# Kernel tuning notes

Hardware: AMD Instinct MI355X
Metric: run time of the kernel (lower is better)

## Reference

```python
import jax, jax.numpy as jnp
import numpy as np

BETA = 0.25
NUM_BOOKS = 8
CODEBOOK_SIZE = 1024
CODEBOOK_DIM = 128
INPUT_DIM = 512


def setup_inputs() -> dict:
    key = jax.random.key(0)
    ks = jax.random.split(key, 6)
    B, T = 16, 4096
    z = jax.random.normal(ks[0], (B, INPUT_DIM, T), dtype=jnp.float32)
    W_in = jax.random.normal(ks[1], (CODEBOOK_DIM, INPUT_DIM), dtype=jnp.float32) * (1.0 / np.sqrt(INPUT_DIM))
    b_in = jax.random.normal(ks[2], (CODEBOOK_DIM,), dtype=jnp.float32) * 0.01
    W_out = jax.random.normal(ks[3], (INPUT_DIM, CODEBOOK_DIM), dtype=jnp.float32) * (1.0 / np.sqrt(CODEBOOK_DIM))
    b_out = jax.random.normal(ks[4], (INPUT_DIM,), dtype=jnp.float32) * 0.01
    # codebooks init: uniform(-1/size, 1/size) as in _make_codebook
    codebooks = jax.random.uniform(ks[5], (NUM_BOOKS, CODEBOOK_SIZE, CODEBOOK_DIM),
                                   dtype=jnp.float32,
                                   minval=-1.0 / CODEBOOK_SIZE, maxval=1.0 / CODEBOOK_SIZE)
    return {"z": z, "W_in": W_in, "b_in": b_in, "W_out": W_out, "b_out": b_out, "codebooks": codebooks}


def reference(z, W_in, b_in, W_out, b_out, codebooks):
    # z: [B, D_in, T]; codebooks: [K_books, S, d]
    residual = z
    total_loss = jnp.float32(0.0)
    codes_list = []
    for i in range(codebooks.shape[0]):
        r = residual.transpose(0, 2, 1)                       # [B, T, D_in]
        z_proj = jnp.einsum('btD,dD->btd', r, W_in) + b_in    # [B, T, d]
        cb = codebooks[i]                                      # [S, d]
        # squared euclidean distance; argmin matches torch.cdist argmin
        d2 = (jnp.sum(z_proj * z_proj, axis=-1, keepdims=True)
              - 2.0 * jnp.einsum('btd,sd->bts', z_proj, cb)
              + jnp.sum(cb * cb, axis=-1))                    # [B, T, S]
        idx = jnp.argmin(d2, axis=-1)                          # [B, T]
        z_q_proj = cb[idx]                                     # [B, T, d] gather
        z_q_st = z_proj + jax.lax.stop_gradient(z_q_proj - z_proj)
        commit = jnp.mean((jax.lax.stop_gradient(z_q_proj) - z_proj) ** 2)
        cb_loss = jnp.mean((z_q_proj - jax.lax.stop_gradient(z_proj)) ** 2)
        total_loss = total_loss + cb_loss + BETA * commit
        z_q = (jnp.einsum('btd,Dd->btD', z_q_st, W_out) + b_out).transpose(0, 2, 1)  # [B, D_in, T]
        residual = residual - z_q
        codes_list.append(idx)
    z_quantized = z - residual
    codes = jnp.stack(codes_list, axis=1)                      # [B, num_books, T]
    return z_quantized, codes, total_loss
```

## Files before the change

### kernel.cpp

```cpp
#include <hip/hip_runtime.h>
#include <cstdint>

constexpr int NB   = 8;
constexpr int S    = 1024;
constexpr int CD   = 128;
constexpr int DIN  = 512;
constexpr int BATCH= 16;
constexpr int T    = 4096;
constexpr int NTOK = BATCH * T;
constexpr int FCAP = 24;
constexpr float MARGIN = 4e-3f;

typedef __attribute__((ext_vector_type(8))) short bf16x8;
typedef __attribute__((ext_vector_type(4))) float f32x4;

__device__ __forceinline__ unsigned short f2bf(float f) {
  unsigned int u = __float_as_uint(f);
  return (unsigned short)((u + 0x7fffu + ((u >> 16) & 1u)) >> 16);
}
__device__ __forceinline__ unsigned int fenc(float f) {
  unsigned int u = __float_as_uint(f);
  return (u & 0x80000000u) ? ~u : (u | 0x80000000u);
}
__device__ __forceinline__ float fdec(unsigned int e) {
  return (e & 0x80000000u) ? __uint_as_float(e ^ 0x80000000u) : __uint_as_float(~e);
}

__global__ __launch_bounds__(256) void cbn32_kernel(const float* __restrict__ cbs,
                                                    float* __restrict__ cbn32) {
  int row = blockIdx.x * 256 + threadIdx.x;
  if (row >= NB * S) return;
  const float4* r4 = reinterpret_cast<const float4*>(cbs + (size_t)row * CD);
  double s = 0.0;
  for (int q = 0; q < 32; ++q) {
    float4 v = r4[q];
    s += (double)v.x * v.x + (double)v.y * v.y + (double)v.z * v.z + (double)v.w * v.w;
  }
  cbn32[row] = (float)s;
}

__global__ __launch_bounds__(256) void cb16_kernel(const float* __restrict__ cbs,
                                                   unsigned short* __restrict__ cb16) {
  int i = blockIdx.x * 256 + threadIdx.x;
  if (i < NB * S * CD) cb16[i] = f2bf(cbs[i]);
}

__global__ __launch_bounds__(256) void p64t_kernel(const float* __restrict__ Win,
                                                   const float* __restrict__ Wout,
                                                   double* __restrict__ P64t) {
  int n = blockIdx.x * 256 + threadIdx.x;
  int k = n >> 7, d = n & 127;
  double s = 0.0;
  for (int D = 0; D < DIN; ++D)
    s = fma((double)Win[(size_t)d * DIN + D], (double)Wout[(size_t)D * CD + k], s);
  P64t[(size_t)k * CD + d] = s;
}

__global__ void cvec64_kernel(const float* __restrict__ Win,
                              const float* __restrict__ bout,
                              double* __restrict__ cvec64) {
  int d = threadIdx.x;
  double s = 0.0;
  for (int D = 0; D < DIN; ++D)
    s = fma((double)Win[(size_t)d * DIN + D], (double)bout[D], s);
  cvec64[d] = s;
}

__global__ void pcf_kernel(const float* __restrict__ cbs,
                           const double* __restrict__ P64t,
                           const double* __restrict__ cvec64,
                           float* __restrict__ PCF32) {
  const int s = blockIdx.x, book = blockIdx.y;
  const int d = threadIdx.x;
  const float* cr = cbs + ((size_t)book * S + s) * CD;
  double acc = 0.0;
  for (int k = 0; k < CD; ++k)
    acc = fma((double)cr[k], P64t[(size_t)k * CD + d], acc);
  PCF32[((size_t)book * S + s) * CD + d] = (float)(acc + cvec64[d]);
}

__global__ __launch_bounds__(256) void winT_kernel(const float* __restrict__ Win,
                                                   float* __restrict__ WinT) {
  int i = blockIdx.x * 256 + threadIdx.x;
  int D = i >> 7, d = i & 127;
  WinT[(size_t)D * 128 + d] = Win[(size_t)d * 512 + D];
}

__global__ __launch_bounds__(256) void woutT_kernel(const float* __restrict__ Wout,
                                                    float* __restrict__ WoutT) {
  int i = blockIdx.x * 256 + threadIdx.x;
  int k = i >> 9, D = i & 511;
  WoutT[(size_t)k * 512 + D] = Wout[(size_t)D * 128 + k];
}

__global__ __launch_bounds__(256) void a32_kernel(const float* __restrict__ z,
                                                  const float* __restrict__ WinT,
                                                  const float* __restrict__ bin,
                                                  float* __restrict__ Acur) {
  __shared__ __align__(16) float Al[32][132];
  __shared__ __align__(16) float Bl[32][68];
  const int tid = threadIdx.x;
  const int t0 = blockIdx.x * 64;
  const int b  = blockIdx.y;
  const int mx = tid & 15, nx = tid >> 4;
  float acc[8][4] = {};
  for (int kc = 0; kc < 16; ++kc) {
    __syncthreads();
#pragma unroll
    for (int rep = 0; rep < 4; ++rep) {
      int idx = rep * 256 + tid;
      int kk = idx >> 5, q = idx & 31;
      float4 v = *reinterpret_cast<const float4*>(WinT + (size_t)(kc * 32 + kk) * 128 + q * 4);
      *reinterpret_cast<float4*>(&Al[kk][q * 4]) = v;
    }
#pragma unroll
    for (int rep = 0; rep < 2; ++rep) {
      int idx = rep * 256 + tid;
      int kk = idx >> 4, q = idx & 15;
      float4 v = reinterpret_cast<const float4*>(z + ((size_t)(b * DIN + kc * 32 + kk)) * T + t0)[q];
      *reinterpret_cast<float4*>(&Bl[kk][q * 4]) = v;
    }
    __syncthreads();
#pragma unroll
    for (int kk = 0; kk < 32; ++kk) {
      float4 a0 = *reinterpret_cast<const float4*>(&Al[kk][mx * 8]);
      float4 a1 = *reinterpret_cast<const float4*>(&Al[kk][mx * 8 + 4]);
      float4 bv = *reinterpret_cast<const float4*>(&Bl[kk][nx * 4]);
      float a[8] = {a0.x, a0.y, a0.z, a0.w, a1.x, a1.y, a1.z, a1.w};
      float bb[4] = {bv.x, bv.y, bv.z, bv.w};
#pragma unroll
      for (int u = 0; u < 8; ++u)
#pragma unroll
        for (int j = 0; j < 4; ++j) acc[u][j] = fmaf(a[u], bb[j], acc[u][j]);
    }
  }
#pragma unroll
  for (int u = 0; u < 8; ++u) {
    int d = mx * 8 + u;
    float bi = bin[d];
    size_t base = (size_t)d * NTOK + (size_t)b * T + t0 + nx * 4;
    float4 o = make_float4(acc[u][0] + bi, acc[u][1] + bi, acc[u][2] + bi, acc[u][3] + bi);
    *reinterpret_cast<float4*>(Acur + base) = o;
  }
}

template <bool LAST>
__global__ __launch_bounds__(256) void fused_kernel(
    float* __restrict__ Acur,
    const unsigned short* __restrict__ cb16b,
    const float* __restrict__ cbb,
    const float* __restrict__ cbn32b,
    const float* __restrict__ PCFb,
    int* __restrict__ codes,
    double* __restrict__ lpartF,
    int book) {
  __shared__ __align__(16) unsigned char smemU[32768];
  __shared__ float Cna[1024];
  __shared__ unsigned int gminU[64];
  __shared__ int   fcnt[64];
  __shared__ unsigned short fls[64][FCAP];
  __shared__ double znp[4][64];
  __shared__ float znl[64];
  __shared__ float bestv[4][64];
  __shared__ int   bests[4][64];
  __shared__ int   ovl[64];
  __shared__ unsigned char ovf[64];
  __shared__ double lred[64];
  __shared__ int   scode[64];
  __shared__ int   ovn;

  auto ZtT = reinterpret_cast<unsigned short(*)[152]>(smemU);

  const int tid = threadIdx.x;
  const int tok0 = blockIdx.x * 64;
  const int wv = tid >> 6, ln = tid & 63;
  const int lr = ln & 15, lg = ln >> 4;

  const unsigned short* abase = cb16b + (size_t)(wv * 32 + lr) * 128 + lg * 8;

  for (int rep = 0; rep < 8; ++rep) {
    int idx = rep * 256 + tid;
    int k = idx >> 4, qq = idx & 15;
    float4 v = *reinterpret_cast<const float4*>(Acur + (size_t)k * NTOK + tok0 + qq * 4);
    ZtT[qq * 4 + 0][k] = f2bf(v.x);
    ZtT[qq * 4 + 1][k] = f2bf(v.y);
    ZtT[qq * 4 + 2][k] = f2bf(v.z);
    ZtT[qq * 4 + 3][k] = f2bf(v.w);
  }
#pragma unroll
  for (int rep = 0; rep < 4; ++rep) Cna[rep * 256 + tid] = cbn32b[rep * 256 + tid];
  if (tid < 64) { gminU[tid] = 0xFFFFFFFFu; fcnt[tid] = 0; }
  __syncthreads();

  {
    bf16x8 pa[8];
#pragma unroll
    for (int ks = 0; ks < 4; ++ks) {
      pa[ks * 2 + 0] = *reinterpret_cast<const bf16x8*>(abase + (size_t)ks * 32);
      pa[ks * 2 + 1] = *reinterpret_cast<const bf16x8*>(abase + 16 * 128 + (size_t)ks * 32);
    }
    for (int c = 0; c < 8; ++c) {
      bf16x8 ca[8];
#pragma unroll
      for (int i = 0; i < 8; ++i) ca[i] = pa[i];
      if (c < 7) {
        const unsigned short* nb = abase + (size_t)(c + 1) * 128 * 128;
#pragma unroll
        for (int ks = 0; ks < 4; ++ks) {
          pa[ks * 2 + 0] = *reinterpret_cast<const bf16x8*>(nb + (size_t)ks * 32);
          pa[ks * 2 + 1] = *reinterpret_cast<const bf16x8*>(nb + 16 * 128 + (size_t)ks * 32);
        }
      }
      f32x4 acc[2][4];
#pragma unroll
      for (int ss = 0; ss < 2; ++ss)
#pragma unroll
        for (int ts = 0; ts < 4; ++ts) acc[ss][ts] = (f32x4){0.f, 0.f, 0.f, 0.f};
#pragma unroll
      for (int ks = 0; ks < 4; ++ks) {
        bf16x8 b0 = *reinterpret_cast<const bf16x8*>(&ZtT[lr][ks * 32 + lg * 8]);
        bf16x8 b1 = *reinterpret_cast<const bf16x8*>(&ZtT[16 + lr][ks * 32 + lg * 8]);
        bf16x8 b2 = *reinterpret_cast<const bf16x8*>(&ZtT[32 + lr][ks * 32 + lg * 8]);
        bf16x8 b3 = *reinterpret_cast<const bf16x8*>(&ZtT[48 + lr][ks * 32 + lg * 8]);
        acc[0][0] = __builtin_amdgcn_mfma_f32_16x16x32_bf16(ca[ks*2+0], b0, acc[0][0], 0, 0, 0);
        acc[0][1] = __builtin_amdgcn_mfma_f32_16x16x32_bf16(ca[ks*2+0], b1, acc[0][1], 0, 0, 0);
        acc[0][2] = __builtin_amdgcn_mfma_f32_16x16x32_bf16(ca[ks*2+0], b2, acc[0][2], 0, 0, 0);
        acc[0][3] = __builtin_amdgcn_mfma_f32_16x16x32_bf16(ca[ks*2+0], b3, acc[0][3], 0, 0, 0);
        acc[1][0] = __builtin_amdgcn_mfma_f32_16x16x32_bf16(ca[ks*2+1], b0, acc[1][0], 0, 0, 0);
        acc[1][1] = __builtin_amdgcn_mfma_f32_16x16x32_bf16(ca[ks*2+1], b1, acc[1][1], 0, 0, 0);
        acc[1][2] = __builtin_amdgcn_mfma_f32_16x16x32_bf16(ca[ks*2+1], b2, acc[1][2], 0, 0, 0);
        acc[1][3] = __builtin_amdgcn_mfma_f32_16x16x32_bf16(ca[ks*2+1], b3, acc[1][3], 0, 0, 0);
      }
#pragma unroll
      for (int ss = 0; ss < 2; ++ss)
#pragma unroll
        for (int ts = 0; ts < 4; ++ts)
#pragma unroll
          for (int r = 0; r < 4; ++r)
            acc[ss][ts][r] = fmaf(-2.f, acc[ss][ts][r],
                                  Cna[c * 128 + wv * 32 + ss * 16 + lg * 4 + r]);
#pragma unroll
      for (int ts = 0; ts < 4; ++ts) {
        float m = acc[0][ts][0];
#pragma unroll
        for (int r = 1; r < 4; ++r) m = fminf(m, acc[0][ts][r]);
#pragma unroll
        for (int r = 0; r < 4; ++r) m = fminf(m, acc[1][ts][r]);
        m = fminf(m, __shfl_xor(m, 16));
        m = fminf(m, __shfl_xor(m, 32));
        if (lg == 0) atomicMin(&gminU[ts * 16 + lr], fenc(m));
      }
    }
  }
  __syncthreads();

  {
    bf16x8 pa[8];
#pragma unroll
    for (int ks = 0; ks < 4; ++ks) {
      pa[ks * 2 + 0] = *reinterpret_cast<const bf16x8*>(abase + (size_t)ks * 32);
      pa[ks * 2 + 1] = *reinterpret_cast<const bf16x8*>(abase + 16 * 128 + (size_t)ks * 32);
    }
    for (int c = 0; c < 8; ++c) {
      bf16x8 ca[8];
#pragma unroll
      for (int i = 0; i < 8; ++i) ca[i] = pa[i];
      if (c < 7) {
        const unsigned short* nb = abase + (size_t)(c + 1) * 128 * 128;
#pragma unroll
        for (int ks = 0; ks < 4; ++ks) {
          pa[ks * 2 + 0] = *reinterpret_cast<const bf16x8*>(nb + (size_t)ks * 32);
          pa[ks * 2 + 1] = *reinterpret_cast<const bf16x8*>(nb + 16 * 128 + (size_t)ks * 32);
        }
      }
      f32x4 acc[2][4];
#pragma unroll
      for (int ss = 0; ss < 2; ++ss)
#pragma unroll
        for (int ts = 0; ts < 4; ++ts) acc[ss][ts] = (f32x4){0.f, 0.f, 0.f, 0.f};
#pragma unroll
      for (int ks = 0; ks < 4; ++ks) {
        bf16x8 b0 = *reinterpret_cast<const bf16x8*>(&ZtT[lr][ks * 32 + lg * 8]);
        bf16x8 b1 = *reinterpret_cast<const bf16x8*>(&ZtT[16 + lr][ks * 32 + lg * 8]);
        bf16x8 b2 = *reinterpret_cast<const bf16x8*>(&ZtT[32 + lr][ks * 32 + lg * 8]);
        bf16x8 b3 = *reinterpret_cast<const bf16x8*>(&ZtT[48 + lr][ks * 32 + lg * 8]);
        acc[0][0] = __builtin_amdgcn_mfma_f32_16x16x32_bf16(ca[ks*2+0], b0, acc[0][0], 0, 0, 0);
        acc[0][1] = __builtin_amdgcn_mfma_f32_16x16x32_bf16(ca[ks*2+0], b1, acc[0][1], 0, 0, 0);
        acc[0][2] = __builtin_amdgcn_mfma_f32_16x16x32_bf16(ca[ks*2+0], b2, acc[0][2], 0, 0, 0);
        acc[0][3] = __builtin_amdgcn_mfma_f32_16x16x32_bf16(ca[ks*2+0], b3, acc[0][3], 0, 0, 0);
        acc[1][0] = __builtin_amdgcn_mfma_f32_16x16x32_bf16(ca[ks*2+1], b0, acc[1][0], 0, 0, 0);
        acc[1][1] = __builtin_amdgcn_mfma_f32_16x16x32_bf16(ca[ks*2+1], b1, acc[1][1], 0, 0, 0);
        acc[1][2] = __builtin_amdgcn_mfma_f32_16x16x32_bf16(ca[ks*2+1], b2, acc[1][2], 0, 0, 0);
        acc[1][3] = __builtin_amdgcn_mfma_f32_16x16x32_bf16(ca[ks*2+1], b3, acc[1][3], 0, 0, 0);
      }
#pragma unroll
      for (int ss = 0; ss < 2; ++ss)
#pragma unroll
        for (int ts = 0; ts < 4; ++ts)
#pragma unroll
          for (int r = 0; r < 4; ++r)
            acc[ss][ts][r] = fmaf(-2.f, acc[ss][ts][r],
                                  Cna[c * 128 + wv * 32 + ss * 16 + lg * 4 + r]);
#pragma unroll
      for (int ts = 0; ts < 4; ++ts) {
        int t = ts * 16 + lr;
        float thr = fdec(gminU[t]) + MARGIN;
#pragma unroll
        for (int ss = 0; ss < 2; ++ss)
#pragma unroll
          for (int r = 0; r < 4; ++r) {
            float v = acc[ss][ts][r];
            if (v <= thr) {
              int s = c * 128 + wv * 32 + ss * 16 + lg * 4 + r;
              int pos = atomicAdd(&fcnt[t], 1);
              if (pos < FCAP) fls[t][pos] = (unsigned short)s;
            }
          }
      }
    }
  }
  __syncthreads();

  auto Zl = reinterpret_cast<float(*)[64]>(smemU);
  float* rm = &bestv[0][0];
  int*   ri = &bests[0][0];

  const int b = tok0 >> 12;
  const int tl = tid & 63, h = tid >> 6;
  if (tid == 0) ovn = 0;
  for (int rep = 0; rep < 8; ++rep) {
    int idx = rep * 256 + tid;
    int d = idx >> 4, q = idx & 15;
    float4 v = *reinterpret_cast<const float4*>(Acur + (size_t)d * NTOK + tok0 + q * 4);
    Zl[d][q * 4 + 0] = v.x; Zl[d][q * 4 + 1] = v.y;
    Zl[d][q * 4 + 2] = v.z; Zl[d][q * 4 + 3] = v.w;
  }
  __syncthreads();
  {
    double s = 0.0;
#pragma unroll
    for (int dd = 0; dd < 32; ++dd) { double v = (double)Zl[h * 32 + dd][tl]; s += v * v; }
    znp[h][tl] = s;
  }
  __syncthreads();
  if (tid < 64) znl[tid] = (float)(((znp[0][tid] + znp[1][tid]) + znp[2][tid]) + znp[3][tid]);
  __syncthreads();
  const float zn = znl[tl];
  const int cnt = fcnt[tl];
  float bm = 3.4e38f; int bi = 0x7fffffff;
  if (cnt <= FCAP) {
    if (h == 0) ovf[tl] = 0;
    for (int i = h; i < cnt; i += 4) {
      int s = fls[tl][i];
      const float* cr = cbb + (size_t)s * CD;
      double e = 0.0;
      for (int d = 0; d < CD; ++d) e = fma((double)cr[d], (double)Zl[d][tl], e);
      float M = (float)e;
      float d2 = __fadd_rn(__fsub_rn(zn, __fmul_rn(2.f, M)), Cna[s]);
      if (d2 < bm || (d2 == bm && s < bi)) { bm = d2; bi = s; }
    }
  } else {
    if (h == 0) { int p = atomicAdd(&ovn, 1); ovl[p] = tl; ovf[tl] = 1; }
  }
  bestv[h][tl] = bm; bests[h][tl] = bi;
  __syncthreads();
  if (tid < 64 && !ovf[tid]) {
    float fv = bestv[0][tid]; int fs = bests[0][tid];
#pragma unroll
    for (int x = 1; x < 4; ++x) {
      float v = bestv[x][tid]; int s = bests[x][tid];
      if (v < fv || (v == fv && s < fs)) { fv = v; fs = s; }
    }
    codes[((size_t)b * NB + book) * T + ((tok0 + tid) & (T - 1))] = fs;
    scode[tid] = fs;
    lred[tid] = (double)fv;
  }
  __syncthreads();
  const int no = ovn;
  for (int e = 0; e < no; ++e) {
    const int tt = ovl[e];
    const float zn2 = znl[tt];
    double e0 = 0.0, e1 = 0.0, e2 = 0.0, e3 = 0.0;
    const float* c0 = cbb + (size_t)(tid      ) * CD;
    const float* c1 = cbb + (size_t)(tid + 256) * CD;
    const float* c2 = cbb + (size_t)(tid + 512) * CD;
    const float* c3 = cbb + (size_t)(tid + 768) * CD;
    for (int d = 0; d < CD; ++d) {
      double zv = (double)Zl[d][tt];
      e0 = fma((double)c0[d], zv, e0);
      e1 = fma((double)c1[d], zv, e1);
      e2 = fma((double)c2[d], zv, e2);
      e3 = fma((double)c3[d], zv, e3);
    }
    float bm2 = 3.4e38f; int bi2 = 0x7fffffff;
    {
      float d2;
      d2 = __fadd_rn(__fsub_rn(zn2, __fmul_rn(2.f, (float)e0)), Cna[tid]);
      if (d2 < bm2) { bm2 = d2; bi2 = tid; }
      d2 = __fadd_rn(__fsub_rn(zn2, __fmul_rn(2.f, (float)e1)), Cna[tid + 256]);
      if (d2 < bm2) { bm2 = d2; bi2 = tid + 256; }
      d2 = __fadd_rn(__fsub_rn(zn2, __fmul_rn(2.f, (float)e2)), Cna[tid + 512]);
      if (d2 < bm2) { bm2 = d2; bi2 = tid + 512; }
      d2 = __fadd_rn(__fsub_rn(zn2, __fmul_rn(2.f, (float)e3)), Cna[tid + 768]);
      if (d2 < bm2) { bm2 = d2; bi2 = tid + 768; }
    }
    rm[tid] = bm2; ri[tid] = bi2;
    __syncthreads();
    for (int off = 128; off; off >>= 1) {
      if (tid < off) {
        float om = rm[tid + off]; int oi = ri[tid + off];
        if (om < rm[tid] || (om == rm[tid] && oi < ri[tid])) { rm[tid] = om; ri[tid] = oi; }
      }
      __syncthreads();
    }
    if (tid == 0) {
      codes[((size_t)b * NB + book) * T + ((tok0 + tt) & (T - 1))] = ri[0];
      scode[tt] = ri[0];
      lred[tt] = (double)rm[0];
    }
    __syncthreads();
  }
  if (tid == 0) {
    double sum = 0.0;
    for (int i = 0; i < 64; ++i) sum += lred[i];
    lpartF[(size_t)book * 1024 + blockIdx.x] = sum;
  }

  if constexpr (!LAST) {
    __syncthreads();
    const int code = scode[tl];
    const float* pr = PCFb + (size_t)code * CD + h * 32;
#pragma unroll
    for (int d = 0; d < 32; ++d) {
      int dd = h * 32 + d;
      Acur[(size_t)dd * NTOK + tok0 + tl] = Zl[dd][tl] - pr[d];
    }
  }
}

__global__ __launch_bounds__(256) void qsgather_kernel(const float* __restrict__ cbs,
                                                       const int* __restrict__ codes,
                                                       float* __restrict__ qs32) {
  __shared__ int cds[64][8];
  const int tid = threadIdx.x;
  const int tok0 = blockIdx.x * 64;
  const int tl = tid & 63, h = tid >> 6;
  if (tid < 64) {
    int tok = tok0 + tid, b = tok >> 12, t = tok & (T - 1);
#pragma unroll
    for (int book = 0; book < NB; ++book)
      cds[tid][book] = codes[((size_t)b * NB + book) * T + t];
  }
  __syncthreads();
  const int tok = tok0 + tl;
  float acc[32] = {};
#pragma unroll
  for (int book = 0; book < NB; ++book) {
    const float* cr = cbs + ((size_t)book * S + cds[tl][book]) * CD + h * 32;
#pragma unroll
    for (int k = 0; k < 32; ++k) acc[k] += cr[k];
  }
#pragma unroll
  for (int k = 0; k < 32; ++k)
    qs32[(size_t)(h * 32 + k) * NTOK + tok] = acc[k];
}

__global__ __launch_bounds__(256) void final32_kernel(const float* __restrict__ qs32,
                                                      const float* __restrict__ WoutT,
                                                      const float* __restrict__ bout,
                                                      float* __restrict__ out) {
  __shared__ __align__(16) float Al[32][132];
  __shared__ __align__(16) float Bl[32][68];
  const int tid = threadIdx.x;
  const int t0 = blockIdx.x * 64;
  const int Dg = blockIdx.y;
  const int b  = blockIdx.z;
  const int mx = tid & 15, nx = tid >> 4;
  const size_t tokbase = (size_t)b * T + t0;
  float acc[8][4] = {};
  for (int kc = 0; kc < 4; ++kc) {
    __syncthreads();
#pragma unroll
    for (int rep = 0; rep < 4; ++rep) {
      int idx = rep * 256 + tid;
      int kk = idx >> 5, q = idx & 31;
      float4 v = *reinterpret_cast<const float4*>(
          WoutT + (size_t)(kc * 32 + kk) * 512 + Dg * 128 + q * 4);
      *reinterpret_cast<float4*>(&Al[kk][q * 4]) = v;
    }
#pragma unroll
    for (int rep = 0; rep < 2; ++rep) {
      int idx = rep * 256 + tid;
      int kk = idx >> 4, q = idx & 15;
      *reinterpret_cast<float4*>(&Bl[kk][q * 4]) =
          *reinterpret_cast<const float4*>(qs32 + (size_t)(kc * 32 + kk) * NTOK + tokbase + q * 4);
    }
    __syncthreads();
#pragma unroll
    for (int kk = 0; kk < 32; ++kk) {
      float4 a0 = *reinterpret_cast<const float4*>(&Al[kk][mx * 8]);
      float4 a1 = *reinterpret_cast<const float4*>(&Al[kk][mx * 8 + 4]);
      float4 bv = *reinterpret_cast<const float4*>(&Bl[kk][nx * 4]);
      float a[8] = {a0.x, a0.y, a0.z, a0.w, a1.x, a1.y, a1.z, a1.w};
      float bb[4] = {bv.x, bv.y, bv.z, bv.w};
#pragma unroll
      for (int u = 0; u < 8; ++u)
#pragma unroll
        for (int j = 0; j < 4; ++j) acc[u][j] = fmaf(a[u], bb[j], acc[u][j]);
    }
  }
#pragma unroll
  for (int u = 0; u < 8; ++u) {
    int D = Dg * 128 + mx * 8 + u;
    float bo = 8.0f * bout[D];
    float4 o = make_float4(acc[u][0] + bo, acc[u][1] + bo, acc[u][2] + bo, acc[u][3] + bo);
    reinterpret_cast<float4*>(out + ((size_t)b * DIN + D) * T + t0)[nx] = o;
  }
}

__global__ __launch_bounds__(256) void codes_out_kernel(const int* __restrict__ codes,
                                                        float* __restrict__ out) {
  int k = blockIdx.x * 256 + threadIdx.x;
  if (k < BATCH * NB * T)
    out[(size_t)BATCH * DIN * T + k] = (float)codes[k];
}

__global__ __launch_bounds__(256) void loss_out_kernel(const double* __restrict__ lpF,
                                                       float* __restrict__ out) {
  __shared__ double red[256];
  double s = 0.0;
  for (int i = threadIdx.x; i < NB * 1024; i += 256) s += lpF[i];
  red[threadIdx.x] = s;
  __syncthreads();
  for (int off = 128; off; off >>= 1) {
    if (threadIdx.x < off) red[threadIdx.x] += red[threadIdx.x + off];
    __syncthreads();
  }
  if (threadIdx.x == 0)
    out[(size_t)BATCH * DIN * T + (size_t)BATCH * NB * T] =
        (float)(red[0] * 1.25 / 8388608.0);
}

extern "C" void kernel_launch(void* const* d_in, const int* in_sizes, int n_in,
                              void* d_out, int out_size, void* d_ws, size_t ws_size,
                              hipStream_t stream) {
  (void)in_sizes; (void)n_in; (void)out_size; (void)ws_size;
  const float* z    = (const float*)d_in[0];
  const float* Win  = (const float*)d_in[1];
  const float* bin  = (const float*)d_in[2];
  const float* Wout = (const float*)d_in[3];
  const float* bout = (const float*)d_in[4];
  const float* cbs  = (const float*)d_in[5];
  float* out = (float*)d_out;
  float* Acur = out;

  char* w = (char*)d_ws;
  double* P64t  = (double*)w;  w += (size_t)CD * CD * 8;
  double* cvec64= (double*)w;  w += CD * 8;
  double* lpartF= (double*)w;  w += (size_t)NB * 1024 * 8;
  float*  PCF32 = (float*)w;   w += (size_t)NB * S * CD * 4;
  float*  qs32  = (float*)w;   w += (size_t)CD * NTOK * 4;
  float*  cbn32 = (float*)w;   w += (size_t)NB * S * 4;
  float*  WinT  = (float*)w;   w += (size_t)DIN * CD * 4;
  float*  WoutT = (float*)w;   w += (size_t)CD * DIN * 4;
  unsigned short* cb16 = (unsigned short*)w; w += (size_t)NB * S * CD * 2;
  int*    codes = (int*)w;     w += (size_t)BATCH * NB * T * 4;

  cbn32_kernel<<<(NB * S + 255) / 256, 256, 0, stream>>>(cbs, cbn32);
  cb16_kernel<<<(NB * S * CD + 255) / 256, 256, 0, stream>>>(cbs, cb16);
  p64t_kernel<<<64, 256, 0, stream>>>(Win, Wout, P64t);
  cvec64_kernel<<<1, 128, 0, stream>>>(Win, bout, cvec64);
  pcf_kernel<<<dim3(S, NB), 128, 0, stream>>>(cbs, P64t, cvec64, PCF32);
  winT_kernel<<<256, 256, 0, stream>>>(Win, WinT);
  woutT_kernel<<<256, 256, 0, stream>>>(Wout, WoutT);
  a32_kernel<<<dim3(T / 64, BATCH), 256, 0, stream>>>(z, WinT, bin, Acur);

  for (int book = 0; book < NB; ++book) {
    const float* cb = cbs + (size_t)book * S * CD;
    const unsigned short* cbh = cb16 + (size_t)book * S * CD;
    if (book < NB - 1)
      fused_kernel<false><<<NTOK / 64, 256, 0, stream>>>(
          Acur, cbh, cb, cbn32 + book * S,
          PCF32 + (size_t)book * S * CD, codes, lpartF, book);
    else
      fused_kernel<true><<<NTOK / 64, 256, 0, stream>>>(
          Acur, cbh, cb, cbn32 + book * S,
          PCF32 + (size_t)book * S * CD, codes, lpartF, book);
  }
  qsgather_kernel<<<NTOK / 64, 256, 0, stream>>>(cbs, codes, qs32);
  final32_kernel<<<dim3(T / 64, DIN / 128, BATCH), 256, 0, stream>>>(qs32, WoutT, bout, out);
  codes_out_kernel<<<(BATCH * NB * T + 255) / 256, 256, 0, stream>>>(codes, out);
  loss_out_kernel<<<1, 256, 0, stream>>>(lpartF, out);
}
```

Baseline: 1.164 ms.

## Fuse candidate filtering into the min pass instead of recomputing distances

Removes the second full pass that recomputed the bf16 MFMA distances for all 1024 codewords. Candidates are now filtered inside the first pass against a running per-token minimum, with a barrier between the min update and the filter. Because the threshold is not yet final for early chunks, more candidates pass, so the per-token candidate capacity grows from 24 to 32. The main risk is overflowing that capacity; a __syncthreads inside the per-chunk loop also adds a barrier per chunk.

Result: slower. 1.199 ms (+3.1%).

```diff
diff --git a/kernel.cpp b/kernel.cpp
--- a/kernel.cpp
+++ b/kernel.cpp
@@ -8,7 +8,7 @@
 constexpr int BATCH= 16;
 constexpr int T    = 4096;
 constexpr int NTOK = BATCH * T;
-constexpr int FCAP = 24;
+constexpr int FCAP = 32;
 constexpr float MARGIN = 4e-3f;
 
 typedef __attribute__((ext_vector_type(8))) short bf16x8;
@@ -250,57 +250,7 @@
         m = fminf(m, __shfl_xor(m, 32));
         if (lg == 0) atomicMin(&gminU[ts * 16 + lr], fenc(m));
       }
-    }
-  }
-  __syncthreads();
-
-  {
-    bf16x8 pa[8];
-#pragma unroll
-    for (int ks = 0; ks < 4; ++ks) {
-      pa[ks * 2 + 0] = *reinterpret_cast<const bf16x8*>(abase + (size_t)ks * 32);
-      pa[ks * 2 + 1] = *reinterpret_cast<const bf16x8*>(abase + 16 * 128 + (size_t)ks * 32);
-    }
-    for (int c = 0; c < 8; ++c) {
-      bf16x8 ca[8];
-#pragma unroll
-      for (int i = 0; i < 8; ++i) ca[i] = pa[i];
-      if (c < 7) {
-        const unsigned short* nb = abase + (size_t)(c + 1) * 128 * 128;
-#pragma unroll
-        for (int ks = 0; ks < 4; ++ks) {
-          pa[ks * 2 + 0] = *reinterpret_cast<const bf16x8*>(nb + (size_t)ks * 32);
-          pa[ks * 2 + 1] = *reinterpret_cast<const bf16x8*>(nb + 16 * 128 + (size_t)ks * 32);
-        }
-      }
-      f32x4 acc[2][4];
-#pragma unroll
-      for (int ss = 0; ss < 2; ++ss)
-#pragma unroll
-        for (int ts = 0; ts < 4; ++ts) acc[ss][ts] = (f32x4){0.f, 0.f, 0.f, 0.f};
-#pragma unroll
-      for (int ks = 0; ks < 4; ++ks) {
-        bf16x8 b0 = *reinterpret_cast<const bf16x8*>(&ZtT[lr][ks * 32 + lg * 8]);
-        bf16x8 b1 = *reinterpret_cast<const bf16x8*>(&ZtT[16 + lr][ks * 32 + lg * 8]);
-        bf16x8 b2 = *reinterpret_cast<const bf16x8*>(&ZtT[32 + lr][ks * 32 + lg * 8]);
-        bf16x8 b3 = *reinterpret_cast<const bf16x8*>(&ZtT[48 + lr][ks * 32 + lg * 8]);
-        acc[0][0] = __builtin_amdgcn_mfma_f32_16x16x32_bf16(ca[ks*2+0], b0, acc[0][0], 0, 0, 0);
-        acc[0][1] = __builtin_amdgcn_mfma_f32_16x16x32_bf16(ca[ks*2+0], b1, acc[0][1], 0, 0, 0);
-        acc[0][2] = __builtin_amdgcn_mfma_f32_16x16x32_bf16(ca[ks*2+0], b2, acc[0][2], 0, 0, 0);
-        acc[0][3] = __builtin_amdgcn_mfma_f32_16x16x32_bf16(ca[ks*2+0], b3, acc[0][3], 0, 0, 0);
-        acc[1][0] = __builtin_amdgcn_mfma_f32_16x16x32_bf16(ca[ks*2+1], b0, acc[1][0], 0, 0, 0);
-        acc[1][1] = __builtin_amdgcn_mfma_f32_16x16x32_bf16(ca[ks*2+1], b1, acc[1][1], 0, 0, 0);
-        acc[1][2] = __builtin_amdgcn_mfma_f32_16x16x32_bf16(ca[ks*2+1], b2, acc[1][2], 0, 0, 0);
-        acc[1][3] = __builtin_amdgcn_mfma_f32_16x16x32_bf16(ca[ks*2+1], b3, acc[1][3], 0, 0, 0);
-      }
-#pragma unroll
-      for (int ss = 0; ss < 2; ++ss)
-#pragma unroll
-        for (int ts = 0; ts < 4; ++ts)
-#pragma unroll
-          for (int r = 0; r < 4; ++r)
-            acc[ss][ts][r] = fmaf(-2.f, acc[ss][ts][r],
-                                  Cna[c * 128 + wv * 32 + ss * 16 + lg * 4 + r]);
+      __syncthreads();
 #pragma unroll
       for (int ts = 0; ts < 4; ++ts) {
         int t = ts * 16 + lr;
```
